# Kernel tuning notes

Measured on AMD Instinct MI355X. Metric: run time of the kernel, lower is better.

Reference implementation:

```python
import jax, jax.numpy as jnp
import numpy as np

N, T, V, C = 64, 64, 64, 64   # batch, time(=ref_channels), joints(=kpt_channels), in_channels
RED, OUT = 2, 64              # red_channels, out_channels


def setup_inputs() -> dict:
    key = jax.random.key(0)
    ks = jax.random.split(key, 8)
    s_m = (2.0 / C) ** 0.5          # kaiming-ish scale for 1x1 convs
    s_rm = (2.0 / (RED * T)) ** 0.5
    s_f = (1.0 / C) ** 0.5
    return {
        "x": jax.random.normal(ks[0], (N, T, V, C), dtype=jnp.float32),
        "A": jax.random.normal(ks[1], (T, V, V), dtype=jnp.float32) * 0.1,
        "w_m1": jax.random.normal(ks[2], (RED, C), dtype=jnp.float32) * s_m,
        "b_m1": jnp.zeros((RED,), dtype=jnp.float32),
        "w_m2": jax.random.normal(ks[3], (RED, C), dtype=jnp.float32) * s_m,
        "b_m2": jnp.zeros((RED,), dtype=jnp.float32),
        "w_rm": jax.random.normal(ks[4], (T, RED * T), dtype=jnp.float32) * s_rm,
        "b_rm": jnp.zeros((T,), dtype=jnp.float32),
        "w_f": jax.random.normal(ks[5], (OUT, C), dtype=jnp.float32) * s_f,
        "b_f": jnp.zeros((OUT,), dtype=jnp.float32),
        "alpha_m": 1,
    }


def reference(x, A, w_m1, b_m1, w_m2, b_m2, w_rm, b_rm, w_f, b_f, alpha_m):
    n = x.shape[0]
    # conv_f: pointwise Linear over channels -> (N,T,V,OUT)
    xf = jnp.einsum('ntvc,oc->ntvo', x, w_f) + b_f
    # conv_m1/conv_m2: 1x1 Conv2d over channel dim -> (N,RED,T,V)
    xm1 = jnp.einsum('ntvc,rc->nrtv', x, w_m1) + b_m1[None, :, None, None]
    xm2 = jnp.einsum('ntvc,rc->nrtv', x, w_m2) + b_m2[None, :, None, None]
    xm1 = xm1.reshape(n, RED * T, V)
    xm2 = xm2.reshape(n, RED * T, V)
    # pairwise outer difference + tanh -> (N, RED*T, V, V)
    xm = jnp.tanh(xm1[..., :, None] - xm2[..., None, :])
    # conv_rm: 1x1 conv reducing RED*T -> T channels, then scale + static adjacency
    adj = jnp.einsum('nkij,tk->ntij', xm, w_rm) + b_rm[None, :, None, None]
    adj = adj * alpha_m + A[None]          # (N,T,V,V)
    # batched matmul: dynamic adjacency x features
    out = jnp.einsum('ntij,ntjo->ntio', adj, xf)  # (N,T,V,OUT)
    return out
```

## Files before the change

### kernel.cpp

```cpp
#include <hip/hip_runtime.h>
#include <hip/hip_bf16.h>


typedef float  f32x4  __attribute__((ext_vector_type(4)));
typedef short  bf16x8 __attribute__((ext_vector_type(8)));
typedef short  bf16x4 __attribute__((ext_vector_type(4)));

static __device__ __forceinline__ short f2bf(float f) {
    __hip_bfloat16 h = __float2bfloat16(f);
    return *reinterpret_cast<short*>(&h);
}

static __device__ __forceinline__ float bf2f(short s) {
    return __uint_as_float(((unsigned)(unsigned short)s) << 16);
}

static __device__ __forceinline__ bf16x8 cvt8f(const float4 a, const float4 b) {
    bf16x8 r;
    r[0] = f2bf(a.x); r[1] = f2bf(a.y); r[2] = f2bf(a.z); r[3] = f2bf(a.w);
    r[4] = f2bf(b.x); r[5] = f2bf(b.y); r[6] = f2bf(b.z); r[7] = f2bf(b.w);
    return r;
}

static __device__ __forceinline__ bf16x8 cvt8(const float* p) {
    return cvt8f(*(const float4*)p, *(const float4*)(p + 4));
}

static __device__ __forceinline__ float tanh_fast(float x) {
    float e = __expf(2.0f * x);
    return 1.0f - 2.0f * __builtin_amdgcn_rcpf(e + 1.0f);
}

static __device__ __forceinline__ float dot4(float4 a, float4 b) {
    return a.x * b.x + a.y * b.y + a.z * b.z + a.w * b.w;
}

static __device__ __forceinline__ float alpha_decode(const int* p) {
    int raw = p[0];
    unsigned ur = (unsigned)(raw < 0 ? -raw : raw);
    return (ur < (1u << 23)) ? (float)raw : __int_as_float(raw);
}

static __device__ __forceinline__ bf16x8 fuse8(bf16x8 s, float4 a0, float4 a1,
                                               float ab) {
    bf16x8 r;
    r[0] = f2bf(bf2f(s[0]) + a0.x + ab);
    r[1] = f2bf(bf2f(s[1]) + a0.y + ab);
    r[2] = f2bf(bf2f(s[2]) + a0.z + ab);
    r[3] = f2bf(bf2f(s[3]) + a0.w + ab);
    r[4] = f2bf(bf2f(s[4]) + a1.x + ab);
    r[5] = f2bf(bf2f(s[5]) + a1.y + ab);
    r[6] = f2bf(bf2f(s[6]) + a1.z + ab);
    r[7] = f2bf(bf2f(s[7]) + a1.w + ab);
    return r;
}

#define MFMA16(a, b, c) __builtin_amdgcn_mfma_f32_16x16x32_bf16((a), (b), (c), 0, 0, 0)

__global__ __launch_bounds__(512) void k0_proj(
    const float* __restrict__ x,
    const float* __restrict__ w_m1, const float* __restrict__ b_m1,
    const float* __restrict__ w_m2, const float* __restrict__ b_m2,
    float* __restrict__ m1T, float* __restrict__ m2T)
{
    __shared__ float msT[4][8][68];

    const int b   = blockIdx.x;
    const int n   = b >> 3;
    const int v0  = (b & 7) * 8;
    const int tid = threadIdx.x;
    const int tl  = tid >> 6;
    const int vv  = (tid >> 3) & 7;
    const int cg  = tid & 7;
    const int c0  = cg * 8;

    const float4 w10 = *(const float4*)(w_m1 + c0);
    const float4 w11 = *(const float4*)(w_m1 + c0 + 4);
    const float4 w20 = *(const float4*)(w_m1 + 64 + c0);
    const float4 w21 = *(const float4*)(w_m1 + 64 + c0 + 4);
    const float4 w30 = *(const float4*)(w_m2 + c0);
    const float4 w31 = *(const float4*)(w_m2 + c0 + 4);
    const float4 w40 = *(const float4*)(w_m2 + 64 + c0);
    const float4 w41 = *(const float4*)(w_m2 + 64 + c0 + 4);

#pragma unroll 2
    for (int it = 0; it < 8; ++it) {
        const int t = it * 8 + tl;
        const size_t R = ((size_t)(n * 64 + t)) * 64 + (v0 + vv);
        const float* xp = x + (R << 6) + c0;
        const float4 a0 = *(const float4*)xp;
        const float4 a1 = *(const float4*)(xp + 4);

        float s0 = dot4(a0, w10) + dot4(a1, w11);
        float s1 = dot4(a0, w20) + dot4(a1, w21);
        float s2 = dot4(a0, w30) + dot4(a1, w31);
        float s3 = dot4(a0, w40) + dot4(a1, w41);

#pragma unroll
        for (int m = 1; m < 8; m <<= 1) {
            s0 += __shfl_xor(s0, m);
            s1 += __shfl_xor(s1, m);
            s2 += __shfl_xor(s2, m);
            s3 += __shfl_xor(s3, m);
        }
        if (cg < 4) {
            float s = (cg == 0) ? s0 : (cg == 1) ? s1 : (cg == 2) ? s2 : s3;
            msT[cg][vv][t] = s;
        }
    }
    __syncthreads();

    {
        const int m   = tid >> 8;
        const int rem = tid & 255;
        const int vv2 = rem >> 5;
        const int k0  = (rem & 31) * 4;
        const int r   = k0 >> 6;
        const int sel = m * 2 + r;
        const int t0  = k0 & 63;
        float4 val = *(const float4*)&msT[sel][vv2][t0];
        const float bias = (m == 0) ? b_m1[r] : b_m2[r];
        val.x += bias; val.y += bias; val.z += bias; val.w += bias;
        float* dst = ((m == 0) ? m1T : m2T) + n * 8192 + (v0 + vv2) * 128 + k0;
        *(float4*)dst = val;
    }
}

__global__ __launch_bounds__(512) void k1_adj(
    const float* __restrict__ w_rm,
    const float* __restrict__ m1T,  const float* __restrict__ m2T,
    const int* __restrict__ alpha_p,
    short* __restrict__ adjm)
{
    __shared__ float m2s[64 * 132];
    __shared__ short wrs[64 * 132];

    const int b   = blockIdx.x;
    const int n   = b >> 3;
    const int i0  = (b & 7) * 8;
    const int tid = threadIdx.x;
    const int l = tid & 63, w = tid >> 6;
    const int lr = l & 15, lg = l >> 4;
    const int ig = i0 + w;

    const float alpha = alpha_decode(alpha_p);

    float4 m1r[8];
#pragma unroll
    for (int kt = 0; kt < 4; ++kt) {
        const float* p = m1T + n * 8192 + ig * 128 + kt * 32 + lg * 8;
        m1r[kt * 2 + 0] = *(const float4*)p;
        m1r[kt * 2 + 1] = *(const float4*)(p + 4);
    }

    {
        const float4* src = (const float4*)(m2T + n * 8192);
        for (int it = tid; it < 2048; it += 512) {
            int j = it >> 5, q = it & 31;
            *(float4*)(m2s + j * 132 + q * 4) = src[it];
        }
    }
    {
        const float4* src = (const float4*)w_rm;
        for (int it = tid; it < 2048; it += 512) {
            int t = it >> 5, q = it & 31;
            float4 v = src[it];
            bf16x4 pv;
            pv[0] = f2bf(alpha * v.x);
            pv[1] = f2bf(alpha * v.y);
            pv[2] = f2bf(alpha * v.z);
            pv[3] = f2bf(alpha * v.w);
            *(bf16x4*)(wrs + t * 132 + q * 4) = pv;
        }
    }
    __syncthreads();

    bf16x8 bfr[4][4];
#pragma unroll
    for (int jt = 0; jt < 4; ++jt) {
        const float* m2row = m2s + (jt * 16 + lr) * 132;
#pragma unroll
        for (int kt = 0; kt < 4; ++kt) {
            const int k0 = kt * 32 + lg * 8;
            float4 b0 = *(const float4*)(m2row + k0);
            float4 b1 = *(const float4*)(m2row + k0 + 4);
            float4 a0 = m1r[kt * 2], a1 = m1r[kt * 2 + 1];
            bfr[jt][kt][0] = f2bf(tanh_fast(a0.x - b0.x));
            bfr[jt][kt][1] = f2bf(tanh_fast(a0.y - b0.y));
            bfr[jt][kt][2] = f2bf(tanh_fast(a0.z - b0.z));
            bfr[jt][kt][3] = f2bf(tanh_fast(a0.w - b0.w));
            bfr[jt][kt][4] = f2bf(tanh_fast(a1.x - b1.x));
            bfr[jt][kt][5] = f2bf(tanh_fast(a1.y - b1.y));
            bfr[jt][kt][6] = f2bf(tanh_fast(a1.z - b1.z));
            bfr[jt][kt][7] = f2bf(tanh_fast(a1.w - b1.w));
        }
    }

    short* adjb = adjm + ((size_t)n << 18) + (ig << 6);

#pragma unroll 1
    for (int q = 0; q < 4; ++q) {
        const int tq = q * 16 + lr;
        bf16x8 af[4];
#pragma unroll
        for (int kt = 0; kt < 4; ++kt)
            af[kt] = *(const bf16x8*)(wrs + tq * 132 + kt * 32 + lg * 8);
        short* tqb = adjb + ((size_t)tq << 12) + lg * 4;
#pragma unroll
        for (int jt = 0; jt < 4; ++jt) {
            f32x4 acc = (f32x4){0.f, 0.f, 0.f, 0.f};
#pragma unroll
            for (int kt = 0; kt < 4; ++kt)
                acc = MFMA16(bfr[jt][kt], af[kt], acc);
            bf16x4 pv;
            pv[0] = f2bf(acc[0]);
            pv[1] = f2bf(acc[1]);
            pv[2] = f2bf(acc[2]);
            pv[3] = f2bf(acc[3]);
            *(bf16x4*)(tqb + jt * 16) = pv;
        }
    }
}

__global__ __launch_bounds__(256) void k2_out(
    const short* __restrict__ adjm, const float* __restrict__ x,
    const float* __restrict__ Ast,  const float* __restrict__ b_rm,
    const int* __restrict__ alpha_p,
    const float* __restrict__ w_f,  const float* __restrict__ b_f,
    float* __restrict__ out)
{
    __shared__ short adjs[64 * 72];
    __shared__ short xT[64 * 72 + 32];
    __shared__ short P[64 * 104];

    const int b   = blockIdx.x;
    const int tid = threadIdx.x;
    const int l = tid & 63, w = tid >> 6;
    const int lr = l & 15, lg = l >> 4;

    const float alpha = alpha_decode(alpha_p);

    const int row0 = tid >> 3;
    const int row1 = row0 + 32;
    const int c8   = (tid & 7) * 8;
    const int jx   = tid >> 2;
    const int cx0  = (tid & 3) * 16;
    const int gx0  = (cx0 >> 4) * 8;

    const int o = w * 16 + lr;
    bf16x8 afw[3];
#pragma unroll
    for (int ks = 0; ks < 2; ++ks)
        afw[ks] = cvt8(w_f + o * 64 + ks * 32 + lg * 8);
    {
        bf16x8 ab2 = {0, 0, 0, 0, 0, 0, 0, 0};
        if (lg == 0) ab2[0] = f2bf(b_f[o]);
        afw[2] = ab2;
    }
    bf16x8 ones = {0, 0, 0, 0, 0, 0, 0, 0};
    if (lr == 0) {
#pragma unroll
        for (int d = 0; d < 8; ++d) ones[d] = (short)0x3F80;
    }

    bf16x8 sA, sB;
    float4 aA0, aA1, aB0, aB1;
    float4 px0, px1, px2, px3;
    float  ab;

    {
        const int p = 4 * b, t = p & 63;
        const short* Ab = adjm + ((size_t)p << 12);
        const float* At = Ast  + ((size_t)t << 12);
        const float* Xb = x    + ((size_t)p << 12);
        sA  = *(const bf16x8*)(Ab + row0 * 64 + c8);
        aA0 = *(const float4*)(At + row0 * 64 + c8);
        aA1 = *(const float4*)(At + row0 * 64 + c8 + 4);
        sB  = *(const bf16x8*)(Ab + row1 * 64 + c8);
        aB0 = *(const float4*)(At + row1 * 64 + c8);
        aB1 = *(const float4*)(At + row1 * 64 + c8 + 4);
        px0 = *(const float4*)(Xb + jx * 64 + cx0);
        px1 = *(const float4*)(Xb + jx * 64 + cx0 + 4);
        px2 = *(const float4*)(Xb + jx * 64 + cx0 + 8);
        px3 = *(const float4*)(Xb + jx * 64 + cx0 + 12);
        ab  = alpha * b_rm[t];
    }
    {
        bf16x8 xrA = cvt8f(px0, px1);
        bf16x8 xrB = cvt8f(px2, px3);
        *(bf16x8*)(adjs + row0 * 72 + c8) = fuse8(sA, aA0, aA1, ab);
        *(bf16x8*)(adjs + row1 * 72 + c8) = fuse8(sB, aB0, aB1, ab);
#pragma unroll
        for (int d = 0; d < 8; ++d) {
            xT[(cx0 + d) * 72 + gx0 + jx]     = xrA[d];
            xT[(cx0 + 8 + d) * 72 + gx0 + jx] = xrB[d];
        }
    }
    if (tid < 128) {
        int row = tid >> 1, cz = 80 + (tid & 1) * 8;
        bf16x8 z = {0, 0, 0, 0, 0, 0, 0, 0};
        *(bf16x8*)(P + row * 104 + cz) = z;
    }
    __syncthreads();

#pragma unroll
    for (int pp = 0; pp < 4; ++pp) {
        const int pair = 4 * b + pp;

        bf16x8 adjA[4][2], bx[2];
#pragma unroll
        for (int mt = 0; mt < 4; ++mt)
#pragma unroll
            for (int ks = 0; ks < 2; ++ks)
                adjA[mt][ks] = *(const bf16x8*)(adjs + (mt * 16 + lr) * 72
                                                + ks * 32 + lg * 8);
#pragma unroll
        for (int ks = 0; ks < 2; ++ks)
            bx[ks] = *(const bf16x8*)(xT + (w * 16 + lr) * 72 + w * 8
                                      + ks * 32 + lg * 8);

        if (pp < 3) {
            const int pn = pair + 1, tn = pn & 63;
            const short* Ab = adjm + ((size_t)pn << 12);
            const float* At = Ast  + ((size_t)tn << 12);
            const float* Xb = x    + ((size_t)pn << 12);
            sA  = *(const bf16x8*)(Ab + row0 * 64 + c8);
            aA0 = *(const float4*)(At + row0 * 64 + c8);
            aA1 = *(const float4*)(At + row0 * 64 + c8 + 4);
            sB  = *(const bf16x8*)(Ab + row1 * 64 + c8);
            aB0 = *(const float4*)(At + row1 * 64 + c8);
            aB1 = *(const float4*)(At + row1 * 64 + c8 + 4);
            px0 = *(const float4*)(Xb + jx * 64 + cx0);
            px1 = *(const float4*)(Xb + jx * 64 + cx0 + 4);
            px2 = *(const float4*)(Xb + jx * 64 + cx0 + 8);
            px3 = *(const float4*)(Xb + jx * 64 + cx0 + 12);
            ab  = alpha * b_rm[tn];
        }

        {
            f32x4 acc[4];
#pragma unroll
            for (int mt = 0; mt < 4; ++mt) acc[mt] = (f32x4){0.f, 0.f, 0.f, 0.f};
#pragma unroll
            for (int ks = 0; ks < 2; ++ks)
#pragma unroll
                for (int mt = 0; mt < 4; ++mt)
                    acc[mt] = MFMA16(adjA[mt][ks], bx[ks], acc[mt]);
#pragma unroll
            for (int mt = 0; mt < 4; ++mt)
#pragma unroll
                for (int e = 0; e < 4; ++e)
                    P[(mt * 16 + lg * 4 + e) * 104 + w * 16 + lr] =
                        f2bf(acc[mt][e]);
            if (w == 0) {
                f32x4 accO[4];
#pragma unroll
                for (int mt = 0; mt < 4; ++mt)
                    accO[mt] = (f32x4){0.f, 0.f, 0.f, 0.f};
#pragma unroll
                for (int ks = 0; ks < 2; ++ks)
#pragma unroll
                    for (int mt = 0; mt < 4; ++mt)
                        accO[mt] = MFMA16(adjA[mt][ks], ones, accO[mt]);
#pragma unroll
                for (int mt = 0; mt < 4; ++mt)
#pragma unroll
                    for (int e = 0; e < 4; ++e)
                        P[(mt * 16 + lg * 4 + e) * 104 + 64 + lr] =
                            f2bf(accO[mt][e]);
            }
        }
        __syncthreads();

        {
            float* Ob = out + ((size_t)pair << 12);
#pragma unroll
            for (int nt = 0; nt < 4; ++nt) {
                const int i = nt * 16 + lr;
                bf16x8 bP[3];
#pragma unroll
                for (int ks = 0; ks < 3; ++ks)
                    bP[ks] = *(const bf16x8*)(P + i * 104 + ks * 32 + lg * 8);
                f32x4 acc = (f32x4){0.f, 0.f, 0.f, 0.f};
#pragma unroll
                for (int ks = 0; ks < 3; ++ks)
                    acc = MFMA16(afw[ks], bP[ks], acc);
                *(f32x4*)(Ob + i * 64 + w * 16 + lg * 4) = acc;
            }
        }
        if (pp < 3) {
            bf16x8 xrA = cvt8f(px0, px1);
            bf16x8 xrB = cvt8f(px2, px3);
            *(bf16x8*)(adjs + row0 * 72 + c8) = fuse8(sA, aA0, aA1, ab);
            *(bf16x8*)(adjs + row1 * 72 + c8) = fuse8(sB, aB0, aB1, ab);
#pragma unroll
            for (int d = 0; d < 8; ++d) {
                xT[(cx0 + d) * 72 + gx0 + jx]     = xrA[d];
                xT[(cx0 + 8 + d) * 72 + gx0 + jx] = xrB[d];
            }
        }
        __syncthreads();
    }
}

extern "C" void kernel_launch(void* const* d_in, const int* in_sizes, int n_in,
                              void* d_out, int out_size, void* d_ws, size_t ws_size,
                              hipStream_t stream)
{
    const float* x    = (const float*)d_in[0];
    const float* A    = (const float*)d_in[1];
    const float* w_m1 = (const float*)d_in[2];
    const float* b_m1 = (const float*)d_in[3];
    const float* w_m2 = (const float*)d_in[4];
    const float* b_m2 = (const float*)d_in[5];
    const float* w_rm = (const float*)d_in[6];
    const float* b_rm = (const float*)d_in[7];
    const float* w_f  = (const float*)d_in[8];
    const float* b_f  = (const float*)d_in[9];
    const int*   alpha = (const int*)d_in[10];

    char* ws = (char*)d_ws;
    short* adjm = (short*)(ws);
    float* m1T = (float*)(ws + (size_t)34 * 1024 * 1024);
    float* m2T = (float*)(ws + (size_t)36 * 1024 * 1024);
    float* out = (float*)d_out;

    k0_proj<<<dim3(512), dim3(512), 0, stream>>>(x, w_m1, b_m1, w_m2, b_m2,
                                                 m1T, m2T);
    k1_adj<<<dim3(512), dim3(512), 0, stream>>>(w_rm, m1T, m2T, alpha, adjm);
    k2_out<<<dim3(1024), dim3(256), 0, stream>>>(adjm, x, A, b_rm, alpha,
                                                 w_f, b_f, out);
}
```

Measured before the change: 64.59 us.

## Stage adjacency tiles in LDS for coalesced 16-byte global stores in k1

k1_adj now uses 1024-thread blocks that each cover 16 rows i, halving the grid. Computed adjacency values are staged in a padded LDS buffer that reuses the m2 staging space through a union. They are then written to global memory as contiguous 16-byte chunks per t-row, replacing scattered 8-byte stores. The cost is extra barriers, higher LDS use per block and fewer blocks, which may reduce occupancy and latency hiding.

```diff
diff --git a/kernel.cpp b/kernel.cpp
--- a/kernel.cpp
+++ b/kernel.cpp
@@ -126,18 +126,21 @@
     }
 }
 
-__global__ __launch_bounds__(512) void k1_adj(
+__global__ __launch_bounds__(1024) void k1_adj(
     const float* __restrict__ w_rm,
     const float* __restrict__ m1T,  const float* __restrict__ m2T,
     const int* __restrict__ alpha_p,
     short* __restrict__ adjm)
 {
-    __shared__ float m2s[64 * 132];
     __shared__ short wrs[64 * 132];
+    __shared__ union {
+        float m2s[64 * 132];
+        short adjL[32 * 1092];
+    } u;
 
     const int b   = blockIdx.x;
-    const int n   = b >> 3;
-    const int i0  = (b & 7) * 8;
+    const int n   = b >> 2;
+    const int i0  = (b & 3) * 16;
     const int tid = threadIdx.x;
     const int l = tid & 63, w = tid >> 6;
     const int lr = l & 15, lg = l >> 4;
@@ -155,14 +158,14 @@
 
     {
         const float4* src = (const float4*)(m2T + n * 8192);
-        for (int it = tid; it < 2048; it += 512) {
+        for (int it = tid; it < 2048; it += 1024) {
             int j = it >> 5, q = it & 31;
-            *(float4*)(m2s + j * 132 + q * 4) = src[it];
+            *(float4*)(u.m2s + j * 132 + q * 4) = src[it];
         }
     }
     {
         const float4* src = (const float4*)w_rm;
-        for (int it = tid; it < 2048; it += 512) {
+        for (int it = tid; it < 2048; it += 1024) {
             int t = it >> 5, q = it & 31;
             float4 v = src[it];
             bf16x4 pv;
@@ -178,7 +181,7 @@
     bf16x8 bfr[4][4];
 #pragma unroll
     for (int jt = 0; jt < 4; ++jt) {
-        const float* m2row = m2s + (jt * 16 + lr) * 132;
+        const float* m2row = u.m2s + (jt * 16 + lr) * 132;
 #pragma unroll
         for (int kt = 0; kt < 4; ++kt) {
             const int k0 = kt * 32 + lg * 8;
@@ -195,30 +198,50 @@
             bfr[jt][kt][7] = f2bf(tanh_fast(a1.w - b1.w));
         }
     }
-
-    short* adjb = adjm + ((size_t)n << 18) + (ig << 6);
+    __syncthreads();
 
 #pragma unroll 1
-    for (int q = 0; q < 4; ++q) {
-        const int tq = q * 16 + lr;
-        bf16x8 af[4];
-#pragma unroll
-        for (int kt = 0; kt < 4; ++kt)
-            af[kt] = *(const bf16x8*)(wrs + tq * 132 + kt * 32 + lg * 8);
-        short* tqb = adjb + ((size_t)tq << 12) + lg * 4;
-#pragma unroll
-        for (int jt = 0; jt < 4; ++jt) {
-            f32x4 acc = (f32x4){0.f, 0.f, 0.f, 0.f};
+    for (int qh = 0; qh < 2; ++qh) {
+#pragma unroll
+        for (int qi = 0; qi < 2; ++qi) {
+            const int q    = 2 * qh + qi;
+            const int tq   = q * 16 + lr;
+            const int tloc = tq - 32 * qh;
+            bf16x8 af[4];
 #pragma unroll
             for (int kt = 0; kt < 4; ++kt)
-                acc = MFMA16(bfr[jt][kt], af[kt], acc);
-            bf16x4 pv;
-            pv[0] = f2bf(acc[0]);
-            pv[1] = f2bf(acc[1]);
-            pv[2] = f2bf(acc[2]);
-            pv[3] = f2bf(acc[3]);
-            *(bf16x4*)(tqb + jt * 16) = pv;
-        }
+                af[kt] = *(const bf16x8*)(wrs + tq * 132 + kt * 32 + lg * 8);
+            short* lbase = u.adjL + tloc * 1092 + w * 68 + lg * 4;
+#pragma unroll
+            for (int jt = 0; jt < 4; ++jt) {
+                f32x4 acc = (f32x4){0.f, 0.f, 0.f, 0.f};
+#pragma unroll
+                for (int kt = 0; kt < 4; ++kt)
+                    acc = MFMA16(bfr[jt][kt], af[kt], acc);
+                bf16x4 pv;
+                pv[0] = f2bf(acc[0]);
+                pv[1] = f2bf(acc[1]);
+                pv[2] = f2bf(acc[2]);
+                pv[3] = f2bf(acc[3]);
+                *(bf16x4*)(lbase + jt * 16) = pv;
+            }
+        }
+        __syncthreads();
+
+        {
+            short* gbase = adjm + ((size_t)n << 18)
+                         + ((size_t)(32 * qh) << 12) + (i0 << 6);
+#pragma unroll
+            for (int it = 0; it < 4; ++it) {
+                const int c   = it * 1024 + tid;
+                const int tl2 = c >> 7;
+                const int il  = (c >> 3) & 15;
+                const int jc  = (c & 7) * 8;
+                bf16x8 v = *(const bf16x8*)(u.adjL + tl2 * 1092 + il * 68 + jc);
+                *(bf16x8*)(gbase + ((size_t)tl2 << 12) + il * 64 + jc) = v;
+            }
+        }
+        __syncthreads();
     }
 }
 
@@ -427,7 +450,7 @@
 
     k0_proj<<<dim3(512), dim3(512), 0, stream>>>(x, w_m1, b_m1, w_m2, b_m2,
                                                  m1T, m2T);
-    k1_adj<<<dim3(512), dim3(512), 0, stream>>>(w_rm, m1T, m2T, alpha, adjm);
+    k1_adj<<<dim3(256), dim3(1024), 0, stream>>>(w_rm, m1T, m2T, alpha, adjm);
     k2_out<<<dim3(1024), dim3(256), 0, stream>>>(adjm, x, A, b_rm, alpha,
                                                  w_f, b_f, out);
 }
```

Result: slower. 67.34 us (+4.3%).
